# Optimization experiments

Measured on AMD Instinct MI355X. Metric: run time of the kernel, lower is better.

Reference implementation:

```python
import jax, jax.numpy as jnp
import numpy as np
from jax import lax

EPS = 1e-5
GROUPS = 8
NUM_HEADS = 8


def setup_inputs() -> dict:
    key = jax.random.key(0)
    ks = jax.random.split(key, 3)
    C = 512
    x = jax.random.normal(ks[0], (8, C, 32, 32), dtype=jnp.float32)
    gamma = jnp.ones((C,), jnp.float32)
    beta = jnp.zeros((C,), jnp.float32)
    w_qkv = jax.random.normal(ks[1], (3 * C, C), dtype=jnp.float32) * (1.0 / np.sqrt(C))
    b_qkv = jnp.zeros((3 * C,), jnp.float32)
    w_proj = jax.random.normal(ks[2], (C, C), dtype=jnp.float32) * (1.0 / np.sqrt(C))
    b_proj = jnp.zeros((C,), jnp.float32)
    return {"x": x, "gamma": gamma, "beta": beta, "w_qkv": w_qkv,
            "b_qkv": b_qkv, "w_proj": w_proj, "b_proj": b_proj}


def reference(x, gamma, beta, w_qkv, b_qkv, w_proj, b_proj):
    b, c, h, w = x.shape
    hd = c // NUM_HEADS
    L = h * w
    # GroupNorm over (c/G, h, w) per group
    xg = x.reshape(b, GROUPS, c // GROUPS, h, w)
    mean = jnp.mean(xg, axis=(2, 3, 4), keepdims=True)
    var = jnp.var(xg, axis=(2, 3, 4), keepdims=True)
    xn = ((xg - mean) * lax.rsqrt(var + EPS)).reshape(b, c, h, w)
    xn = xn * gamma[None, :, None, None] + beta[None, :, None, None]
    # 1x1 conv QKV projection over flattened spatial dim
    xr = xn.reshape(b, c, L)
    qkv = jnp.einsum('oc,bcl->bol', w_qkv, xr) + b_qkv[None, :, None]
    q, k, v = jnp.split(qkv, 3, axis=1)
    # [b, H, L, hd]
    q = q.reshape(b, NUM_HEADS, hd, L).transpose(0, 1, 3, 2)
    k = k.reshape(b, NUM_HEADS, hd, L).transpose(0, 1, 3, 2)
    v = v.reshape(b, NUM_HEADS, hd, L).transpose(0, 1, 3, 2)
    scale = 1.0 / np.sqrt(hd).astype(np.float32)
    attn = jnp.einsum('bhqd,bhkd->bhqk', q, k) * scale
    attn = jax.nn.softmax(attn, axis=-1)
    out = jnp.einsum('bhqk,bhkd->bhqd', attn, v)  # [b, H, L, hd]
    out = out.transpose(0, 1, 3, 2).reshape(b, c, L)
    out = jnp.einsum('oc,bcl->bol', w_proj, out) + b_proj[None, :, None]
    return x + out.reshape(b, c, h, w)
```

## Files before the change

kernel.cpp:

```cpp
#include <hip/hip_runtime.h>
#include <hip/hip_bf16.h>

typedef unsigned short u16;
typedef __attribute__((ext_vector_type(8))) short short8;
typedef __attribute__((ext_vector_type(4))) float floatx4;
typedef __attribute__((ext_vector_type(16))) float floatx16;
typedef __attribute__((ext_vector_type(4))) unsigned uint4v;

struct __attribute__((aligned(8))) u16x4 { u16 x, y, z, w; };
struct __attribute__((aligned(16))) u16x8 { u16 v[8]; };

__device__ __forceinline__ u16 f2bf(float f) {
  unsigned u = __builtin_bit_cast(unsigned, f);
  u += 0x7fff + ((u >> 16) & 1);
  return (u16)(u >> 16);
}

__device__ __forceinline__ unsigned cvt_pk_bf16(float lo, float hi) {
  unsigned d;
  asm("v_cvt_pk_bf16_f32 %0, %1, %2" : "=v"(d) : "v"(lo), "v"(hi));
  return d;
}

__device__ __forceinline__ void gload_lds16(const u16* g, u16* l) {
  __builtin_amdgcn_global_load_lds(
      (const __attribute__((address_space(1))) void*)g,
      (__attribute__((address_space(3))) void*)l, 16, 0, 0);
}

__global__ __launch_bounds__(256) void k_convert(
    const float* __restrict__ wq, const float* __restrict__ wp,
    u16* __restrict__ oq, u16* __restrict__ op) {
  int t = blockIdx.x * 256 + threadIdx.x;
  constexpr int NQ4 = (1536 * 512) / 4;
  constexpr int NP4 = (512 * 512) / 4;
  if (t < NQ4) {
    float4 v = reinterpret_cast<const float4*>(wq)[t];
    u16x4 o = { f2bf(v.x), f2bf(v.y), f2bf(v.z), f2bf(v.w) };
    reinterpret_cast<u16x4*>(oq)[t] = o;
  } else if (t - NQ4 < NP4) {
    int i = t - NQ4;
    float4 v = reinterpret_cast<const float4*>(wp)[i];
    u16x4 o = { f2bf(v.x), f2bf(v.y), f2bf(v.z), f2bf(v.w) };
    reinterpret_cast<u16x4*>(op)[i] = o;
  }
}

__global__ __launch_bounds__(256) void k_gn_stats(const float* __restrict__ x,
                                                  float* __restrict__ stats) {
  int bg = blockIdx.x >> 3, sl = blockIdx.x & 7;
  int b = bg >> 3, g = bg & 7;
  const float* base = x + ((size_t)(b * 512 + g * 64) * 1024) + sl * 128;
  float s = 0.f, ss = 0.f;
#pragma unroll
  for (int i = 0; i < 8; ++i) {
    int idx = threadIdx.x + i * 256;
    int c = idx >> 5, l4 = idx & 31;
    float4 v = *reinterpret_cast<const float4*>(base + (size_t)c * 1024 + l4 * 4);
    s += v.x + v.y + v.z + v.w;
    ss += v.x * v.x + v.y * v.y + v.z * v.z + v.w * v.w;
  }
#pragma unroll
  for (int d = 1; d < 64; d <<= 1) { s += __shfl_xor(s, d); ss += __shfl_xor(ss, d); }
  __shared__ float rs[4], rss[4];
  int wid = threadIdx.x >> 6;
  if ((threadIdx.x & 63) == 0) { rs[wid] = s; rss[wid] = ss; }
  __syncthreads();
  if (threadIdx.x == 0) {
    stats[(bg * 8 + sl) * 2]     = rs[0] + rs[1] + rs[2] + rs[3];
    stats[(bg * 8 + sl) * 2 + 1] = rss[0] + rss[1] + rss[2] + rss[3];
  }
}

__global__ __launch_bounds__(256) void k_gn_norm(
    const float* __restrict__ x, const float* __restrict__ gamma,
    const float* __restrict__ beta, const float* __restrict__ stats,
    u16* __restrict__ xnT) {
  int bg = blockIdx.x >> 3, sl = blockIdx.x & 7;
  int b = bg >> 3, g = bg & 7;
  float s = 0.f, ss = 0.f;
#pragma unroll
  for (int i = 0; i < 8; ++i) { s += stats[(bg * 8 + i) * 2]; ss += stats[(bg * 8 + i) * 2 + 1]; }
  const float inv_n = 1.0f / 65536.0f;
  float mean = s * inv_n;
  float var = ss * inv_n - mean * mean;
  float istd = rsqrtf(var + 1e-5f);
  __shared__ float tile[128 * 65];
  const float* base = x + ((size_t)(b * 512 + g * 64) * 1024) + sl * 128;
#pragma unroll
  for (int i = 0; i < 8; ++i) {
    int idx = threadIdx.x + i * 256;
    int c = idx >> 5, l4 = idx & 31;
    float4 v = *reinterpret_cast<const float4*>(base + (size_t)c * 1024 + l4 * 4);
    float gm = gamma[g * 64 + c];
    float ga = gm * istd;
    float be = beta[g * 64 + c] - mean * ga;
    tile[(l4 * 4 + 0) * 65 + c] = v.x * ga + be;
    tile[(l4 * 4 + 1) * 65 + c] = v.y * ga + be;
    tile[(l4 * 4 + 2) * 65 + c] = v.z * ga + be;
    tile[(l4 * 4 + 3) * 65 + c] = v.w * ga + be;
  }
  __syncthreads();
  u16* obase = xnT + ((size_t)(b * 1024 + sl * 128) * 512) + g * 64;
#pragma unroll
  for (int i = 0; i < 8; ++i) {
    int idx = threadIdx.x + i * 256;
    int l = idx >> 4, c4 = (idx & 15) * 4;
    u16x4 o = { f2bf(tile[l * 65 + c4]),     f2bf(tile[l * 65 + c4 + 1]),
                f2bf(tile[l * 65 + c4 + 2]), f2bf(tile[l * 65 + c4 + 3]) };
    *reinterpret_cast<u16x4*>(obase + (size_t)l * 512 + c4) = o;
  }
}

__global__ __launch_bounds__(512) void k_qkv(
    const u16* __restrict__ A, const u16* __restrict__ Bm,
    const float* __restrict__ bias,
    u16* __restrict__ Qb, u16* __restrict__ Kb, u16* __restrict__ Vb) {
  int nt = blockIdx.x & 7;
  int rem = blockIdx.x >> 3;
  int b = rem & 7;
  int mt = rem >> 3;
  int tid = threadIdx.x;
  int lane = tid & 63, wid = tid >> 6;
  int wm = wid >> 2, wn = wid & 3;

  union SM {
    u16 ab[2][2][128 * 64];
    u16 c16[128 * 136];
  };
  __shared__ SM sm;

  floatx4 acc[4][2];
#pragma unroll
  for (int m = 0; m < 4; ++m)
#pragma unroll
    for (int n = 0; n < 2; ++n) acc[m][n] = floatx4{0.f, 0.f, 0.f, 0.f};

  const u16* Abase = A + (size_t)(mt * 128) * 512;
  const u16* Bbase = Bm + ((size_t)(b * 1024 + nt * 128)) * 512;
  int cb0 = (lane & 7) ^ (lane >> 3);
  const u16* asrc = Abase + (size_t)(wid * 16 + (lane >> 3)) * 512 + cb0 * 8;
  const u16* bsrc = Bbase + (size_t)(wid * 16 + (lane >> 3)) * 512 + cb0 * 8;

#define STAGE(BUF, KK)                                                           \
  {                                                                              \
    _Pragma("unroll")                                                            \
    for (int j = 0; j < 2; ++j) {                                                \
      gload_lds16(asrc + (size_t)j * 8 * 512 + (KK) * 64,                        \
                  &sm.ab[BUF][0][(wid * 16 + j * 8) * 64]);                      \
      gload_lds16(bsrc + (size_t)j * 8 * 512 + (KK) * 64,                        \
                  &sm.ab[BUF][1][(wid * 16 + j * 8) * 64]);                      \
    }                                                                            \
  }

  STAGE(0, 0);
#pragma unroll
  for (int kk = 0; kk < 8; ++kk) {
    const int cur = kk & 1;
    if (kk < 7) {
      STAGE(cur ^ 1, kk + 1);
      asm volatile("s_waitcnt vmcnt(4)" ::: "memory");
    } else {
      asm volatile("s_waitcnt vmcnt(0)" ::: "memory");
    }
    __builtin_amdgcn_s_barrier();
    __builtin_amdgcn_sched_barrier(0);
    const u16* Asc = sm.ab[cur][0];
    const u16* Bsc = sm.ab[cur][1];
#pragma unroll
    for (int kc = 0; kc < 2; ++kc) {
      int cbk = kc * 4 + (lane >> 4);
      short8 af[4], bf[2];
#pragma unroll
      for (int m = 0; m < 4; ++m) {
        int row = wm * 64 + m * 16 + (lane & 15);
        af[m] = *reinterpret_cast<const short8*>(Asc + row * 64 + ((cbk ^ (row & 7)) * 8));
      }
#pragma unroll
      for (int n = 0; n < 2; ++n) {
        int row = wn * 32 + n * 16 + (lane & 15);
        bf[n] = *reinterpret_cast<const short8*>(Bsc + row * 64 + ((cbk ^ (row & 7)) * 8));
      }
      __builtin_amdgcn_s_setprio(1);
#pragma unroll
      for (int m = 0; m < 4; ++m)
#pragma unroll
        for (int n = 0; n < 2; ++n)
          acc[m][n] = __builtin_amdgcn_mfma_f32_16x16x32_bf16(af[m], bf[n], acc[m][n], 0, 0, 0);
      __builtin_amdgcn_s_setprio(0);
    }
    __builtin_amdgcn_s_barrier();
  }
#undef STAGE

  int sec = mt >> 2;
  int ow0 = (mt & 3) * 128;
#pragma unroll
  for (int m = 0; m < 4; ++m) {
#pragma unroll
    for (int n = 0; n < 2; ++n) {
#pragma unroll
      for (int r = 0; r < 4; ++r) {
        int o_l = wm * 64 + m * 16 + ((lane >> 4) * 4) + r;
        int l_l = wn * 32 + n * 16 + (lane & 15);
        float v = acc[m][n][r] + bias[mt * 128 + o_l];
        if (sec == 0) v *= 0.18033688f;
        u16 bv = f2bf(v);
        if (sec < 2) sm.c16[l_l * 136 + o_l] = bv;
        else         sm.c16[o_l * 136 + l_l] = bv;
      }
    }
  }
  __syncthreads();
  u16* dst = (sec == 0) ? Qb : (sec == 1 ? Kb : Vb);
#pragma unroll
  for (int p = 0; p < 4; ++p) {
    int row = p * 32 + (tid >> 4);
    int col = (tid & 15) * 8;
    u16x8 vv = *reinterpret_cast<const u16x8*>(&sm.c16[row * 136 + col]);
    size_t gi;
    if (sec < 2) gi = ((size_t)(b * 1024 + nt * 128 + row)) * 512 + ow0 + col;
    else         gi = ((size_t)(b * 512 + ow0 + row)) * 1024 + nt * 128 + col;
    *reinterpret_cast<u16x8*>(dst + gi) = vv;
  }
}

__global__ __launch_bounds__(256) void k_proj(
    const u16* __restrict__ A, const u16* __restrict__ Bm,
    const float* __restrict__ bias, const float* __restrict__ xres,
    float* __restrict__ out) {
  int nt = blockIdx.x & 7;
  int rem = blockIdx.x >> 3;
  int b = rem & 7;
  int mt = rem >> 3;
  int tid = threadIdx.x;
  int lane = tid & 63, wid = tid >> 6;
  int wm = wid >> 1, wn = wid & 1;

  union SM {
    u16 ab[2][2][128 * 64];
    float c32[128 * 128];
  };
  __shared__ SM sm;

  floatx4 acc[4][4];
#pragma unroll
  for (int m = 0; m < 4; ++m)
#pragma unroll
    for (int n = 0; n < 4; ++n) acc[m][n] = floatx4{0.f, 0.f, 0.f, 0.f};

  const u16* Abase = A + (size_t)(mt * 128) * 512;
  const u16* Bbase = Bm + ((size_t)(b * 1024 + nt * 128)) * 512;
  int cb0 = (lane & 7) ^ (lane >> 3);
  const u16* asrc = Abase + (size_t)(wid * 32 + (lane >> 3)) * 512 + cb0 * 8;
  const u16* bsrc = Bbase + (size_t)(wid * 32 + (lane >> 3)) * 512 + cb0 * 8;

#define PSTAGE(BUF, KK)                                                          \
  {                                                                              \
    _Pragma("unroll")                                                            \
    for (int j = 0; j < 4; ++j) {                                                \
      gload_lds16(asrc + (size_t)j * 8 * 512 + (KK) * 64,                        \
                  &sm.ab[BUF][0][(wid * 32 + j * 8) * 64]);                      \
      gload_lds16(bsrc + (size_t)j * 8 * 512 + (KK) * 64,                        \
                  &sm.ab[BUF][1][(wid * 32 + j * 8) * 64]);                      \
    }                                                                            \
  }

  PSTAGE(0, 0);
#pragma unroll
  for (int kk = 0; kk < 8; ++kk) {
    const int cur = kk & 1;
    if (kk < 7) {
      PSTAGE(cur ^ 1, kk + 1);
      asm volatile("s_waitcnt vmcnt(8)" ::: "memory");
    } else {
      asm volatile("s_waitcnt vmcnt(0)" ::: "memory");
    }
    __builtin_amdgcn_s_barrier();
    __builtin_amdgcn_sched_barrier(0);
    const u16* Asc = sm.ab[cur][0];
    const u16* Bsc = sm.ab[cur][1];
#pragma unroll
    for (int kc = 0; kc < 2; ++kc) {
      int cbk = kc * 4 + (lane >> 4);
      short8 af[4], bf[4];
#pragma unroll
      for (int m = 0; m < 4; ++m) {
        int row = wm * 64 + m * 16 + (lane & 15);
        af[m] = *reinterpret_cast<const short8*>(Asc + row * 64 + ((cbk ^ (row & 7)) * 8));
      }
#pragma unroll
      for (int n = 0; n < 4; ++n) {
        int row = wn * 64 + n * 16 + (lane & 15);
        bf[n] = *reinterpret_cast<const short8*>(Bsc + row * 64 + ((cbk ^ (row & 7)) * 8));
      }
      __builtin_amdgcn_s_setprio(1);
#pragma unroll
      for (int m = 0; m < 4; ++m)
#pragma unroll
        for (int n = 0; n < 4; ++n)
          acc[m][n] = __builtin_amdgcn_mfma_f32_16x16x32_bf16(af[m], bf[n], acc[m][n], 0, 0, 0);
      __builtin_amdgcn_s_setprio(0);
    }
    __builtin_amdgcn_s_barrier();
  }
#undef PSTAGE

#pragma unroll
  for (int m = 0; m < 4; ++m)
#pragma unroll
    for (int n = 0; n < 4; ++n)
#pragma unroll
      for (int r = 0; r < 4; ++r) {
        int o_l = wm * 64 + m * 16 + ((lane >> 4) * 4) + r;
        int l_l = wn * 64 + n * 16 + (lane & 15);
        sm.c32[o_l * 128 + l_l] = acc[m][n][r] + bias[mt * 128 + o_l];
      }
  __syncthreads();
#pragma unroll
  for (int p = 0; p < 16; ++p) {
    int row = p * 8 + (tid >> 5);
    int col = (tid & 31) * 4;
    float4 vv = *reinterpret_cast<const float4*>(&sm.c32[row * 128 + col]);
    size_t gi = ((size_t)(b * 512 + mt * 128 + row)) * 1024 + nt * 128 + col;
    float4 xr = *reinterpret_cast<const float4*>(xres + gi);
    vv.x += xr.x; vv.y += xr.y; vv.z += xr.z; vv.w += xr.w;
    *reinterpret_cast<float4*>(out + gi) = vv;
  }
}

__global__ __launch_bounds__(256) void k_attn(
    const u16* __restrict__ Qb, const u16* __restrict__ Kb,
    const u16* __restrict__ Vb, u16* __restrict__ OT) {
  int qt = blockIdx.x & 7;
  int h = (blockIdx.x >> 3) & 7;
  int b = blockIdx.x >> 6;
  int tid = threadIdx.x;
  int lane = tid & 63, wid = tid >> 6;
  int l31 = lane & 31, g = lane >> 5;
  int r7 = l31 & 7;
  __shared__ u16 Ks[64 * 64], Vs[64 * 64];

  short8 qf[4];
  int qrow = qt * 128 + wid * 32 + l31;
  const u16* qp = Qb + ((size_t)(b * 1024 + qrow)) * 512 + h * 64 + g * 8;
#pragma unroll
  for (int kc2 = 0; kc2 < 4; ++kc2)
    qf[kc2] = *reinterpret_cast<const short8*>(qp + kc2 * 16);

  floatx16 oacc[2];
#pragma unroll
  for (int nd = 0; nd < 2; ++nd)
#pragma unroll
    for (int r = 0; r < 16; ++r) oacc[nd][r] = 0.f;
  float m = -1e30f, se = 0.f;

  const u16* ksrc[2]; const u16* vsrc[2]; int sdst[2];
#pragma unroll
  for (int i = 0; i < 2; ++i) {
    int idx = tid + i * 256;
    int row = idx >> 3, cb = idx & 7;
    ksrc[i] = Kb + ((size_t)(b * 1024 + row)) * 512 + h * 64 + cb * 8;
    vsrc[i] = Vb + ((size_t)(b * 512 + h * 64 + row)) * 1024 + cb * 8;
    sdst[i] = row * 64 + ((cb ^ (row & 7)) * 8);
  }
  short8 kreg[2], vreg[2];
#pragma unroll
  for (int i = 0; i < 2; ++i) {
    kreg[i] = *reinterpret_cast<const short8*>(ksrc[i]);
    vreg[i] = *reinterpret_cast<const short8*>(vsrc[i]);
  }

  for (int kt = 0; kt < 16; ++kt) {
#pragma unroll
    for (int i = 0; i < 2; ++i) {
      *reinterpret_cast<short8*>(Ks + sdst[i]) = kreg[i];
      *reinterpret_cast<short8*>(Vs + sdst[i]) = vreg[i];
    }
    __syncthreads();
    if (kt < 15) {
#pragma unroll
      for (int i = 0; i < 2; ++i) {
        kreg[i] = *reinterpret_cast<const short8*>(ksrc[i] + (size_t)(kt + 1) * 64 * 512);
        vreg[i] = *reinterpret_cast<const short8*>(vsrc[i] + (kt + 1) * 64);
      }
    }
    floatx16 sacc[2];
#pragma unroll
    for (int nk = 0; nk < 2; ++nk)
#pragma unroll
      for (int r = 0; r < 16; ++r) sacc[nk][r] = 0.f;
#pragma unroll
    for (int nk = 0; nk < 2; ++nk) {
      const u16* krow = Ks + (nk * 32 + l31) * 64;
#pragma unroll
      for (int kc2 = 0; kc2 < 4; ++kc2) {
        int cb = kc2 * 2 + g;
        short8 kf = *reinterpret_cast<const short8*>(krow + ((cb ^ r7) * 8));
        sacc[nk] = __builtin_amdgcn_mfma_f32_32x32x16_bf16(kf, qf[kc2], sacc[nk], 0, 0, 0);
      }
    }
    float pmax = sacc[0][0];
#pragma unroll
    for (int r = 1; r < 16; ++r) pmax = fmaxf(pmax, sacc[0][r]);
#pragma unroll
    for (int r = 0; r < 16; ++r) pmax = fmaxf(pmax, sacc[1][r]);
    pmax = fmaxf(pmax, __shfl_xor(pmax, 32));
    if (__any(pmax > m + 8.0f)) {
      float mn = fmaxf(m, pmax);
      float f = __builtin_amdgcn_exp2f(m - mn);
      m = mn;
      se *= f;
#pragma unroll
      for (int nd = 0; nd < 2; ++nd)
#pragma unroll
        for (int r = 0; r < 16; ++r) oacc[nd][r] *= f;
    }
    float sum = 0.f;
#pragma unroll
    for (int nk = 0; nk < 2; ++nk)
#pragma unroll
      for (int r = 0; r < 16; ++r) {
        float pv = __builtin_amdgcn_exp2f(sacc[nk][r] - m);
        sacc[nk][r] = pv;
        sum += pv;
      }
    sum += __shfl_xor(sum, 32);
    se += sum;
#pragma unroll
    for (int nk = 0; nk < 2; ++nk) {
#pragma unroll
      for (int kc = 0; kc < 2; ++kc) {
        int base = kc * 8;
        unsigned w0 = cvt_pk_bf16(sacc[nk][base + 0], sacc[nk][base + 1]);
        unsigned w2 = cvt_pk_bf16(sacc[nk][base + 4], sacc[nk][base + 5]);
        auto s0 = __builtin_amdgcn_permlane32_swap((int)w0, (int)w2, false, false);
        unsigned w1 = cvt_pk_bf16(sacc[nk][base + 2], sacc[nk][base + 3]);
        unsigned w3 = cvt_pk_bf16(sacc[nk][base + 6], sacc[nk][base + 7]);
        auto s1 = __builtin_amdgcn_permlane32_swap((int)w1, (int)w3, false, false);
        short8 pf = __builtin_bit_cast(short8,
            uint4v{(unsigned)s0[0], (unsigned)s1[0], (unsigned)s0[1], (unsigned)s1[1]});
#pragma unroll
        for (int nd = 0; nd < 2; ++nd) {
          const u16* vrow = Vs + (nd * 32 + l31) * 64;
          int cb = nk * 4 + kc * 2 + g;
          short8 vf = *reinterpret_cast<const short8*>(vrow + ((cb ^ r7) * 8));
          oacc[nd] = __builtin_amdgcn_mfma_f32_32x32x16_bf16(vf, pf, oacc[nd], 0, 0, 0);
        }
      }
    }
    __syncthreads();
  }
  float inv = 1.0f / se;
  u16* obase = OT + ((size_t)(b * 1024 + qrow)) * 512 + h * 64;
#pragma unroll
  for (int nd = 0; nd < 2; ++nd) {
#pragma unroll
    for (int rq = 0; rq < 4; ++rq) {
      u16x4 o = { f2bf(oacc[nd][rq * 4 + 0] * inv), f2bf(oacc[nd][rq * 4 + 1] * inv),
                  f2bf(oacc[nd][rq * 4 + 2] * inv), f2bf(oacc[nd][rq * 4 + 3] * inv) };
      *reinterpret_cast<u16x4*>(obase + nd * 32 + rq * 8 + g * 4) = o;
    }
  }
}

extern "C" void kernel_launch(void* const* d_in, const int* in_sizes, int n_in,
                              void* d_out, int out_size, void* d_ws, size_t ws_size,
                              hipStream_t stream) {
  const float* x      = (const float*)d_in[0];
  const float* gamma  = (const float*)d_in[1];
  const float* beta   = (const float*)d_in[2];
  const float* w_qkv  = (const float*)d_in[3];
  const float* b_qkv  = (const float*)d_in[4];
  const float* w_proj = (const float*)d_in[5];
  const float* b_proj = (const float*)d_in[6];
  float* out = (float*)d_out;

  char* ws = (char*)d_ws;
  size_t off = 0;
  float* stats = (float*)(ws + off); off += 4096;
  u16* wqb = (u16*)(ws + off); off += (size_t)1536 * 512 * 2;
  u16* wpb = (u16*)(ws + off); off += (size_t)512 * 512 * 2;
  u16* xnT = (u16*)(ws + off); off += (size_t)8 * 1024 * 512 * 2;
  u16* Qb  = (u16*)(ws + off); off += (size_t)8 * 1024 * 512 * 2;
  u16* Kb  = (u16*)(ws + off); off += (size_t)8 * 1024 * 512 * 2;
  u16* Vb  = (u16*)(ws + off); off += (size_t)8 * 1024 * 512 * 2;
  u16* OT  = (u16*)(ws + off); off += (size_t)8 * 1024 * 512 * 2;
  if (ws_size < off) return;

  k_convert<<<1024, 256, 0, stream>>>(w_qkv, w_proj, wqb, wpb);
  k_gn_stats<<<512, 256, 0, stream>>>(x, stats);
  k_gn_norm<<<512, 256, 0, stream>>>(x, gamma, beta, stats, xnT);
  k_qkv<<<768, 512, 0, stream>>>(wqb, xnT, b_qkv, Qb, Kb, Vb);
  k_attn<<<512, 256, 0, stream>>>(Qb, Kb, Vb, OT);
  k_proj<<<256, 256, 0, stream>>>(wpb, OT, b_proj, x, out);
}
```

Baseline: 86.07 us.

## Store K/V in MFMA fragment order and async double-buffer attention tiles

The QKV GEMM epilogue now writes K and V tiles in a pre-swizzled layout that matches the per-lane MFMA fragment order of the attention kernel. This lets k_attn stream each 64-key tile with contiguous direct global-to-LDS loads into double buffers, replacing the register staging, swizzled LDS writes and __syncthreads. MFMA sections get setprio hints, and nontemporal loads/stores are added for the Q and output writes and the residual read. The risk is layout coupling between the two kernels and more complex index math in the epilogue.

```diff
diff --git a/kernel.cpp b/kernel.cpp
--- a/kernel.cpp
+++ b/kernel.cpp
@@ -26,6 +26,10 @@
   __builtin_amdgcn_global_load_lds(
       (const __attribute__((address_space(1))) void*)g,
       (__attribute__((address_space(3))) void*)l, 16, 0, 0);
+}
+
+__device__ __forceinline__ void nt_store16(u16* p, u16x8 v) {
+  __builtin_nontemporal_store(__builtin_bit_cast(uint4v, v), (uint4v*)p);
 }
 
 __global__ __launch_bounds__(256) void k_convert(
@@ -115,7 +119,7 @@
 __global__ __launch_bounds__(512) void k_qkv(
     const u16* __restrict__ A, const u16* __restrict__ Bm,
     const float* __restrict__ bias,
-    u16* __restrict__ Qb, u16* __restrict__ Kb, u16* __restrict__ Vb) {
+    u16* __restrict__ Qb, u16* __restrict__ Kf, u16* __restrict__ Vf) {
   int nt = blockIdx.x & 7;
   int rem = blockIdx.x >> 3;
   int b = rem & 7;
@@ -142,16 +146,13 @@
   const u16* asrc = Abase + (size_t)(wid * 16 + (lane >> 3)) * 512 + cb0 * 8;
   const u16* bsrc = Bbase + (size_t)(wid * 16 + (lane >> 3)) * 512 + cb0 * 8;
 
-#define STAGE(BUF, KK)                                                           \
-  {                                                                              \
-    _Pragma("unroll")                                                            \
-    for (int j = 0; j < 2; ++j) {                                                \
-      gload_lds16(asrc + (size_t)j * 8 * 512 + (KK) * 64,                        \
-                  &sm.ab[BUF][0][(wid * 16 + j * 8) * 64]);                      \
-      gload_lds16(bsrc + (size_t)j * 8 * 512 + (KK) * 64,                        \
-                  &sm.ab[BUF][1][(wid * 16 + j * 8) * 64]);                      \
-    }                                                                            \
-  }
+  auto STAGE = [&](int BUF, int KK) {
+#pragma unroll
+    for (int j = 0; j < 2; ++j) {
+      gload_lds16(asrc + (size_t)j * 8 * 512 + KK * 64, &sm.ab[BUF][0][(wid * 16 + j * 8) * 64]);
+      gload_lds16(bsrc + (size_t)j * 8 * 512 + KK * 64, &sm.ab[BUF][1][(wid * 16 + j * 8) * 64]);
+    }
+  };
 
   STAGE(0, 0);
 #pragma unroll
@@ -191,10 +192,8 @@
     }
     __builtin_amdgcn_s_barrier();
   }
-#undef STAGE
 
   int sec = mt >> 2;
-  int ow0 = (mt & 3) * 128;
 #pragma unroll
   for (int m = 0; m < 4; ++m) {
 #pragma unroll
@@ -212,16 +211,50 @@
     }
   }
   __syncthreads();
-  u16* dst = (sec == 0) ? Qb : (sec == 1 ? Kb : Vb);
-#pragma unroll
-  for (int p = 0; p < 4; ++p) {
-    int row = p * 32 + (tid >> 4);
-    int col = (tid & 15) * 8;
-    u16x8 vv = *reinterpret_cast<const u16x8*>(&sm.c16[row * 136 + col]);
-    size_t gi;
-    if (sec < 2) gi = ((size_t)(b * 1024 + nt * 128 + row)) * 512 + ow0 + col;
-    else         gi = ((size_t)(b * 512 + ow0 + row)) * 1024 + nt * 128 + col;
-    *reinterpret_cast<u16x8*>(dst + gi) = vv;
+  if (sec == 0) {
+    int ow0 = (mt & 3) * 128;
+#pragma unroll
+    for (int p = 0; p < 4; ++p) {
+      int row = p * 32 + (tid >> 4);
+      int col = (tid & 15) * 8;
+      u16x8 vv = *reinterpret_cast<const u16x8*>(&sm.c16[row * 136 + col]);
+      size_t gi = ((size_t)(b * 1024 + nt * 128 + row)) * 512 + ow0 + col;
+      nt_store16(Qb + gi, vv);
+    }
+  } else if (sec == 1) {
+#pragma unroll
+    for (int p = 0; p < 4; ++p) {
+      int gc = p * 512 + tid;
+      int lane2 = gc & 63;
+      int f = (gc >> 6) & 7;
+      int ht = gc >> 9;
+      int h_loc = ht >> 1, kt_loc = ht & 1;
+      int l_l = kt_loc * 64 + (f >> 2) * 32 + (lane2 & 31);
+      int o_l = h_loc * 64 + (f & 3) * 16 + (lane2 >> 5) * 8;
+      u16x8 vv = *reinterpret_cast<const u16x8*>(&sm.c16[l_l * 136 + o_l]);
+      int hh = (mt & 3) * 2 + h_loc;
+      int kt = nt * 2 + kt_loc;
+      size_t gi = ((((size_t)(b * 8 + hh) * 16 + kt) * 8 + f) * 64 + lane2) * 8;
+      nt_store16(Kf + gi, vv);
+    }
+  } else {
+#pragma unroll
+    for (int p = 0; p < 4; ++p) {
+      int gc = p * 512 + tid;
+      int lane2 = gc & 63;
+      int g2 = lane2 >> 5, l31d = lane2 & 31;
+      int f6 = (gc >> 6) & 7;
+      int ht = gc >> 9;
+      int h_loc = ht >> 1, kt_loc = ht & 1;
+      int nd = f6 & 1, ckc = f6 >> 1;
+      int o_l = h_loc * 64 + nd * 32 + l31d;
+      int l_l = kt_loc * 64 + (ckc * 2 + g2) * 8;
+      u16x8 vv = *reinterpret_cast<const u16x8*>(&sm.c16[o_l * 136 + l_l]);
+      int hh = (mt & 3) * 2 + h_loc;
+      int kt = nt * 2 + kt_loc;
+      size_t gi = ((((size_t)(b * 8 + hh) * 16 + kt) * 8 + f6) * 64 + lane2) * 8;
+      nt_store16(Vf + gi, vv);
+    }
   }
 }
 
@@ -255,16 +288,13 @@
   const u16* asrc = Abase + (size_t)(wid * 32 + (lane >> 3)) * 512 + cb0 * 8;
   const u16* bsrc = Bbase + (size_t)(wid * 32 + (lane >> 3)) * 512 + cb0 * 8;
 
-#define PSTAGE(BUF, KK)                                                          \
-  {                                                                              \
-    _Pragma("unroll")                                                            \
-    for (int j = 0; j < 4; ++j) {                                                \
-      gload_lds16(asrc + (size_t)j * 8 * 512 + (KK) * 64,                        \
-                  &sm.ab[BUF][0][(wid * 32 + j * 8) * 64]);                      \
-      gload_lds16(bsrc + (size_t)j * 8 * 512 + (KK) * 64,                        \
-                  &sm.ab[BUF][1][(wid * 32 + j * 8) * 64]);                      \
-    }                                                                            \
-  }
+  auto PSTAGE = [&](int BUF, int KK) {
+#pragma unroll
+    for (int j = 0; j < 4; ++j) {
+      gload_lds16(asrc + (size_t)j * 8 * 512 + KK * 64, &sm.ab[BUF][0][(wid * 32 + j * 8) * 64]);
+      gload_lds16(bsrc + (size_t)j * 8 * 512 + KK * 64, &sm.ab[BUF][1][(wid * 32 + j * 8) * 64]);
+    }
+  };
 
   PSTAGE(0, 0);
 #pragma unroll
@@ -304,7 +334,6 @@
     }
     __builtin_amdgcn_s_barrier();
   }
-#undef PSTAGE
 
 #pragma unroll
   for (int m = 0; m < 4; ++m)
@@ -321,25 +350,24 @@
   for (int p = 0; p < 16; ++p) {
     int row = p * 8 + (tid >> 5);
     int col = (tid & 31) * 4;
-    float4 vv = *reinterpret_cast<const float4*>(&sm.c32[row * 128 + col]);
+    floatx4 vv = *reinterpret_cast<const floatx4*>(&sm.c32[row * 128 + col]);
     size_t gi = ((size_t)(b * 512 + mt * 128 + row)) * 1024 + nt * 128 + col;
-    float4 xr = *reinterpret_cast<const float4*>(xres + gi);
-    vv.x += xr.x; vv.y += xr.y; vv.z += xr.z; vv.w += xr.w;
-    *reinterpret_cast<float4*>(out + gi) = vv;
+    floatx4 xr = __builtin_nontemporal_load(reinterpret_cast<const floatx4*>(xres + gi));
+    vv += xr;
+    __builtin_nontemporal_store(vv, reinterpret_cast<floatx4*>(out + gi));
   }
 }
 
 __global__ __launch_bounds__(256) void k_attn(
-    const u16* __restrict__ Qb, const u16* __restrict__ Kb,
-    const u16* __restrict__ Vb, u16* __restrict__ OT) {
+    const u16* __restrict__ Qb, const u16* __restrict__ Kf,
+    const u16* __restrict__ Vf, u16* __restrict__ OT) {
   int qt = blockIdx.x & 7;
   int h = (blockIdx.x >> 3) & 7;
   int b = blockIdx.x >> 6;
   int tid = threadIdx.x;
   int lane = tid & 63, wid = tid >> 6;
   int l31 = lane & 31, g = lane >> 5;
-  int r7 = l31 & 7;
-  __shared__ u16 Ks[64 * 64], Vs[64 * 64];
+  __shared__ u16 Ks[2][4096], Vs[2][4096];
 
   short8 qf[4];
   int qrow = qt * 128 + wid * 32 + l31;
@@ -355,51 +383,44 @@
     for (int r = 0; r < 16; ++r) oacc[nd][r] = 0.f;
   float m = -1e30f, se = 0.f;
 
-  const u16* ksrc[2]; const u16* vsrc[2]; int sdst[2];
-#pragma unroll
-  for (int i = 0; i < 2; ++i) {
-    int idx = tid + i * 256;
-    int row = idx >> 3, cb = idx & 7;
-    ksrc[i] = Kb + ((size_t)(b * 1024 + row)) * 512 + h * 64 + cb * 8;
-    vsrc[i] = Vb + ((size_t)(b * 512 + h * 64 + row)) * 1024 + cb * 8;
-    sdst[i] = row * 64 + ((cb ^ (row & 7)) * 8);
-  }
-  short8 kreg[2], vreg[2];
-#pragma unroll
-  for (int i = 0; i < 2; ++i) {
-    kreg[i] = *reinterpret_cast<const short8*>(ksrc[i]);
-    vreg[i] = *reinterpret_cast<const short8*>(vsrc[i]);
-  }
-
+  const u16* kb = Kf + ((size_t)(b * 8 + h) * 16) * 4096;
+  const u16* vb = Vf + ((size_t)(b * 8 + h) * 16) * 4096;
+
+  auto ASTG = [&](int bf, int kt) {
+    const u16* ks = kb + kt * 4096 + tid * 8;
+    const u16* vs = vb + kt * 4096 + tid * 8;
+    gload_lds16(ks,        &Ks[bf][tid * 8]);
+    gload_lds16(ks + 2048, &Ks[bf][2048 + tid * 8]);
+    gload_lds16(vs,        &Vs[bf][tid * 8]);
+    gload_lds16(vs + 2048, &Vs[bf][2048 + tid * 8]);
+  };
+
+  ASTG(0, 0);
   for (int kt = 0; kt < 16; ++kt) {
-#pragma unroll
-    for (int i = 0; i < 2; ++i) {
-      *reinterpret_cast<short8*>(Ks + sdst[i]) = kreg[i];
-      *reinterpret_cast<short8*>(Vs + sdst[i]) = vreg[i];
-    }
-    __syncthreads();
+    const int cur = kt & 1;
     if (kt < 15) {
-#pragma unroll
-      for (int i = 0; i < 2; ++i) {
-        kreg[i] = *reinterpret_cast<const short8*>(ksrc[i] + (size_t)(kt + 1) * 64 * 512);
-        vreg[i] = *reinterpret_cast<const short8*>(vsrc[i] + (kt + 1) * 64);
-      }
-    }
+      ASTG(cur ^ 1, kt + 1);
+      asm volatile("s_waitcnt vmcnt(4)" ::: "memory");
+    } else {
+      asm volatile("s_waitcnt vmcnt(0)" ::: "memory");
+    }
+    __builtin_amdgcn_s_barrier();
+    __builtin_amdgcn_sched_barrier(0);
     floatx16 sacc[2];
 #pragma unroll
     for (int nk = 0; nk < 2; ++nk)
 #pragma unroll
       for (int r = 0; r < 16; ++r) sacc[nk][r] = 0.f;
+    __builtin_amdgcn_s_setprio(1);
 #pragma unroll
     for (int nk = 0; nk < 2; ++nk) {
-      const u16* krow = Ks + (nk * 32 + l31) * 64;
 #pragma unroll
       for (int kc2 = 0; kc2 < 4; ++kc2) {
-        int cb = kc2 * 2 + g;
-        short8 kf = *reinterpret_cast<const short8*>(krow + ((cb ^ r7) * 8));
+        short8 kf = *reinterpret_cast<const short8*>(&Ks[cur][(nk * 4 + kc2) * 512 + lane * 8]);
         sacc[nk] = __builtin_amdgcn_mfma_f32_32x32x16_bf16(kf, qf[kc2], sacc[nk], 0, 0, 0);
       }
     }
+    __builtin_amdgcn_s_setprio(0);
     float pmax = sacc[0][0];
 #pragma unroll
     for (int r = 1; r < 16; ++r) pmax = fmaxf(pmax, sacc[0][r]);
@@ -440,16 +461,17 @@
         auto s1 = __builtin_amdgcn_permlane32_swap((int)w1, (int)w3, false, false);
         short8 pf = __builtin_bit_cast(short8,
             uint4v{(unsigned)s0[0], (unsigned)s1[0], (unsigned)s0[1], (unsigned)s1[1]});
+        __builtin_amdgcn_s_setprio(1);
 #pragma unroll
         for (int nd = 0; nd < 2; ++nd) {
-          const u16* vrow = Vs + (nd * 32 + l31) * 64;
-          int cb = nk * 4 + kc * 2 + g;
-          short8 vf = *reinterpret_cast<const short8*>(vrow + ((cb ^ r7) * 8));
+          short8 vf = *reinterpret_cast<const short8*>(
+              &Vs[cur][(nk * 4 + kc * 2 + nd) * 512 + lane * 8]);
           oacc[nd] = __builtin_amdgcn_mfma_f32_32x32x16_bf16(vf, pf, oacc[nd], 0, 0, 0);
         }
-      }
-    }
-    __syncthreads();
+        __builtin_amdgcn_s_setprio(0);
+      }
+    }
+    __builtin_amdgcn_s_barrier();
   }
   float inv = 1.0f / se;
   u16* obase = OT + ((size_t)(b * 1024 + qrow)) * 512 + h * 64;
@@ -483,15 +505,15 @@
   u16* wpb = (u16*)(ws + off); off += (size_t)512 * 512 * 2;
   u16* xnT = (u16*)(ws + off); off += (size_t)8 * 1024 * 512 * 2;
   u16* Qb  = (u16*)(ws + off); off += (size_t)8 * 1024 * 512 * 2;
-  u16* Kb  = (u16*)(ws + off); off += (size_t)8 * 1024 * 512 * 2;
-  u16* Vb  = (u16*)(ws + off); off += (size_t)8 * 1024 * 512 * 2;
+  u16* Kf  = (u16*)(ws + off); off += (size_t)8 * 1024 * 512 * 2;
+  u16* Vf  = (u16*)(ws + off); off += (size_t)8 * 1024 * 512 * 2;
   u16* OT  = (u16*)(ws + off); off += (size_t)8 * 1024 * 512 * 2;
   if (ws_size < off) return;
 
   k_convert<<<1024, 256, 0, stream>>>(w_qkv, w_proj, wqb, wpb);
   k_gn_stats<<<512, 256, 0, stream>>>(x, stats);
   k_gn_norm<<<512, 256, 0, stream>>>(x, gamma, beta, stats, xnT);
-  k_qkv<<<768, 512, 0, stream>>>(wqb, xnT, b_qkv, Qb, Kb, Vb);
-  k_attn<<<512, 256, 0, stream>>>(Qb, Kb, Vb, OT);
+  k_qkv<<<768, 512, 0, stream>>>(wqb, xnT, b_qkv, Qb, Kf, Vf);
+  k_attn<<<512, 256, 0, stream>>>(Qb, Kf, Vf, OT);
   k_proj<<<256, 256, 0, stream>>>(wpb, OT, b_proj, x, out);
 }
```

After: 94.62 us. 1.1x slower.
